# Kernel tuning notes

Measured on AMD Instinct MI355X. Metric: run time of the kernel, lower is better.

Reference implementation:

```python
import jax, jax.numpy as jnp
import numpy as np

B, L, E, V, H, M, O = 16, 64, 256, 16000, 8, 4, 2
DH = E // H
START = 0

def _pe():
    pos = np.arange(L, dtype=np.float32)[:, None]
    div = np.exp(np.arange(0, E, 2, dtype=np.float32) * (-np.log(10000.0) / E))
    pe = np.zeros((L, E), dtype=np.float32)
    pe[:, 0::2] = np.sin(pos * div)
    pe[:, 1::2] = np.cos(pos * div)
    return jnp.asarray(pe)

PE = _pe()  # [L, E] sinusoidal positional encoding (dropout p=0.0)


def setup_inputs() -> dict:
    key = jax.random.key(0)
    ks = jax.random.split(key, 16)
    g = lambda k, sh, sc: jax.random.normal(k, sh, jnp.float32) * sc
    return {
        'noise': jax.random.normal(ks[0], (B, L), jnp.float32),
        'inEmb_W': g(ks[1], (M, L, L), 1.0 / np.sqrt(L)),   # M stacked Linear(L, L), [in,out] layout
        'inEmb_b': jnp.zeros((M, L), jnp.float32),
        'Wq': g(ks[2], (O, E, E), 1.0 / np.sqrt(E)),
        'bq': jnp.zeros((O, E), jnp.float32),
        'Wk': g(ks[3], (O, E, E), 1.0 / np.sqrt(E)),
        'bk': jnp.zeros((O, E), jnp.float32),
        'Wv': g(ks[4], (O, E, E), 1.0 / np.sqrt(E)),
        'bv': jnp.zeros((O, E), jnp.float32),
        'Wo': g(ks[5], (O, E, E), 1.0 / np.sqrt(E)),
        'bo': jnp.zeros((O, E), jnp.float32),
        'ln_g': jnp.ones((O, E), jnp.float32),
        'ln_b': jnp.zeros((O, E), jnp.float32),
        'emb': g(ks[6], (V, E), 1.0),                       # Word2Vec embedding table
        'soft_W': g(ks[7], (E, V), 1.0 / np.sqrt(E)),       # soft head Linear(E, V)
        'soft_b': jnp.zeros((V,), jnp.float32),
    }


def _ln(x, g, b):
    mu = x.mean(-1, keepdims=True)
    var = ((x - mu) ** 2).mean(-1, keepdims=True)
    return (x - mu) / jnp.sqrt(var + 1e-5) * g + b


def _mha_norm(kv, q, Wq, bq, Wk, bk, Wv, bv, Wo, bo, g, b, kmask):
    # MHAwithNorm: attn(query=q, key=kv, value=kv) -> out proj -> residual -> LayerNorm
    Q = (q @ Wq + bq).reshape(B, L, H, DH)
    K = (kv @ Wk + bk).reshape(B, L, H, DH)
    Vh = (kv @ Wv + bv).reshape(B, L, H, DH)
    s = jnp.einsum('bqhd,bkhd->bhqk', Q, K) / np.sqrt(DH)
    s = jnp.where(kmask[None, None, None, :], s, -1e9)  # only the tok generated positions are valid keys
    a = jax.nn.softmax(s, axis=-1)
    o = jnp.einsum('bhqk,bkhd->bqhd', a, Vh).reshape(B, L, E)
    return _ln(o @ Wo + bo + q, g, b)


def _decode(noise, inEmb_W, inEmb_b, Wq, bq, Wk, bk, Wv, bv, Wo, bo, ln_g, ln_b, emb, soft_W, soft_b):
    w = noise
    for i in range(M):
        w = w @ inEmb_W[i] + inEmb_b[i]
    w = jnp.broadcast_to(w[:, :, None], (B, L, E))  # unsqueeze(-1).repeat(1,1,E)

    Y0 = jnp.zeros((B, L, E), jnp.float32).at[:, 0].set(emb[START] + PE[0])

    def step(Y, tok):
        kmask = jnp.arange(L) < tok  # current sequence length == tok
        out = Y
        for i in range(O):  # cross-attn blocks against w[:, :tok]
            out = _mha_norm(w, out, Wq[i], bq[i], Wk[i], bk[i], Wv[i], bv[i], Wo[i], bo[i], ln_g[i], ln_b[i], kmask)
        for i in range(O):  # same blocks reused as self-attn (faithful to source)
            out = _mha_norm(out, out, Wq[i], bq[i], Wk[i], bk[i], Wv[i], bv[i], Wo[i], bo[i], ln_g[i], ln_b[i], kmask)
        logits = out[:, tok - 1] @ soft_W + soft_b
        probs = jax.nn.softmax(logits, axis=-1)
        nxt = jnp.argmax(probs, axis=-1)  # [B]
        Y = Y.at[:, tok].set(emb[nxt] + PE[tok])
        return Y, (nxt, probs)

    _, (toks, probs) = jax.lax.scan(step, Y0, jnp.arange(1, L))
    return toks, probs  # toks [L-1, B] int, probs [L-1, B, V]


def reference(noise, inEmb_W, inEmb_b, Wq, bq, Wk, bk, Wv, bv, Wo, bo, ln_g, ln_b, emb, soft_W, soft_b):
    toks, _ = _decode(noise, inEmb_W, inEmb_b, Wq, bq, Wk, bk, Wv, bv, Wo, bo, ln_g, ln_b, emb, soft_W, soft_b)
    # torch.stack(out_sent[0]): generated token ids of batch element 0, incl. <START>
    return jnp.concatenate([jnp.array([START], dtype=toks.dtype), toks[:, 0]])
```

## Files before the change

### kernel.cpp

```cpp
#include <hip/hip_runtime.h>
#include <stdint.h>


#define NWG 128
#define NT 256

typedef unsigned long long ull;

__device__ __forceinline__ float ld_c(const float* p){
  return __hip_atomic_load(p, __ATOMIC_RELAXED, __HIP_MEMORY_SCOPE_AGENT);
}
__device__ __forceinline__ void st_c(float* p, float v){
  __hip_atomic_store(p, v, __ATOMIC_RELAXED, __HIP_MEMORY_SCOPE_AGENT);
}
__device__ __forceinline__ int ld_fi(const int* p){
  return __hip_atomic_load(p, __ATOMIC_RELAXED, __HIP_MEMORY_SCOPE_AGENT);
}
__device__ __forceinline__ void st_fi(int* p, int v){
  __hip_atomic_store(p, v, __ATOMIC_RELAXED, __HIP_MEMORY_SCOPE_AGENT);
}
__device__ __forceinline__ ull ld_u64(const ull* p){
  return __hip_atomic_load(p, __ATOMIC_RELAXED, __HIP_MEMORY_SCOPE_AGENT);
}
__device__ __forceinline__ void st_u64(ull* p, ull v){
  __hip_atomic_store(p, v, __ATOMIC_RELAXED, __HIP_MEMORY_SCOPE_AGENT);
}

__device__ __forceinline__ float wredsum(float v){
#pragma unroll
  for (int m=32;m;m>>=1) v += __shfl_xor(v,m,64);
  return v;
}
__device__ __forceinline__ float wredmax(float v){
#pragma unroll
  for (int m=32;m;m>>=1) v = fmaxf(v,__shfl_xor(v,m,64));
  return v;
}
__device__ __forceinline__ float g32sum(float v){
#pragma unroll
  for (int m=16;m;m>>=1) v += __shfl_xor(v,m,64);
  return v;
}
__device__ __forceinline__ float g32max(float v){
#pragma unroll
  for (int m=16;m;m>>=1) v = fmaxf(v,__shfl_xor(v,m,64));
  return v;
}
__device__ __forceinline__ ull shflx64(ull v,int m){
  unsigned int lo=(unsigned int)(v&0xffffffffull), hi=(unsigned int)(v>>32);
  lo=__shfl_xor(lo,m,64); hi=__shfl_xor(hi,m,64);
  return (((ull)hi)<<32)|(ull)lo;
}

__device__ __forceinline__ float pe_val(int l, int e){
  int j = e >> 1;
  float dv = expf((float)(2*j) * (-0.035977892078031970f));
  float arg = (float)l * dv;
  return (e & 1) ? cosf(arg) : sinf(arg);
}

__device__ __forceinline__ void a_chain(const float* xrow, float* rrow,
    float* m8, float* redv,
    const float* KAP, const float* BETA, const float* WVEC,
    const float* CC, const float* UT,
    const float* lng, const float* lnb, int tokm, int t){
  const float ISQ = 0.17677669529663687f;
  for (int blk=0; blk<2; blk++){
    const float* src = blk ? rrow : xrow;
    int hh=t>>5, j=t&31;
    float part=0.f;
    for (int jj=j; jj<256; jj+=32) part += src[jj]*KAP[(blk*8+hh)*256+jj];
    part = g32sum(part);
    float alpha = (part + BETA[blk*8+hh]) * ISQ;
    float s1 = (j<tokm)     ? alpha*WVEC[j]    : -3.4e38f;
    float s2 = (j+32<tokm)  ? alpha*WVEC[j+32] : -3.4e38f;
    float mx = g32max(fmaxf(s1,s2));
    float e1 = expf(s1-mx), e2 = expf(s2-mx);
    float sn = e1*((j<tokm)?WVEC[j]:0.f) + e2*((j+32<tokm)?WVEC[j+32]:0.f);
    float sd = e1+e2;
    sn=g32sum(sn); sd=g32sum(sd);
    if (j==0) m8[hh]=sn/sd;
    __syncthreads();
    float x_ = blk ? rrow[t] : xrow[t];
    float z = CC[blk*256+t] + x_;
#pragma unroll
    for (int h2=0;h2<8;h2++) z += m8[h2]*UT[(blk*8+h2)*256+t];
    float ssum=wredsum(z), ssq=wredsum(z*z);
    int lane=t&63, wid=t>>6;
    if (lane==0){ redv[wid]=ssum; redv[4+wid]=ssq; }
    __syncthreads();
    float ts=redv[0]+redv[1]+redv[2]+redv[3];
    float tq=redv[4]+redv[5]+redv[6]+redv[7];
    float mu=ts*(1.f/256.f);
    float var=tq*(1.f/256.f)-mu*mu;
    float rstd=1.f/sqrtf(var+1e-5f);
    float rv=(z-mu)*rstd*lng[blk*256+t]+lnb[blk*256+t];
    __syncthreads();
    rrow[t]=rv;
    __syncthreads();
  }
}

__device__ __forceinline__ void gbar_f(int* arr, int* rel, int ep){
  __syncthreads();
  if (threadIdx.x==0){
    __builtin_amdgcn_fence(__ATOMIC_RELEASE, "agent");
    __hip_atomic_store(arr + blockIdx.x*16, ep, __ATOMIC_RELAXED, __HIP_MEMORY_SCOPE_AGENT);
  }
  if (blockIdx.x==0){
    if (threadIdx.x < NWG){
      while (__hip_atomic_load(arr + threadIdx.x*16, __ATOMIC_RELAXED, __HIP_MEMORY_SCOPE_AGENT) != ep)
        __builtin_amdgcn_s_sleep(1);
    }
    __syncthreads();
    if (threadIdx.x==0)
      __hip_atomic_store(rel, ep, __ATOMIC_RELAXED, __HIP_MEMORY_SCOPE_AGENT);
  }
  if (threadIdx.x==0){
    while (__hip_atomic_load(rel, __ATOMIC_RELAXED, __HIP_MEMORY_SCOPE_AGENT) != ep)
      __builtin_amdgcn_s_sleep(1);
    __builtin_amdgcn_fence(__ATOMIC_ACQUIRE, "agent");
  }
  __syncthreads();
}

__device__ __forceinline__ void gbar_nf3(int* arr, int* relv, int ep){
  __syncthreads();
  if (threadIdx.x==0)
    st_fi(arr + blockIdx.x*16, ep);
  if (blockIdx.x==0){
    if (threadIdx.x < NWG){
      while (ld_fi(arr + threadIdx.x*16) != ep) __builtin_amdgcn_s_sleep(1);
    }
    __syncthreads();
    if (threadIdx.x < NWG) st_fi(relv + threadIdx.x*16, ep);
  }
  if (threadIdx.x==0){
    while (ld_fi(relv + blockIdx.x*16) != ep) __builtin_amdgcn_s_sleep(1);
  }
  __syncthreads();
}

extern "C" __global__ __launch_bounds__(256, 2)
void gen18124_kernel(const float* __restrict__ noise,
                     const float* __restrict__ iw, const float* __restrict__ ib,
                     const float* __restrict__ Wq, const float* __restrict__ bq,
                     const float* __restrict__ Wk, const float* __restrict__ bk,
                     const float* __restrict__ Wv, const float* __restrict__ bv,
                     const float* __restrict__ Wo, const float* __restrict__ bo,
                     const float* __restrict__ lng, const float* __restrict__ lnb,
                     const float* __restrict__ emb, const float* __restrict__ sw,
                     const float* __restrict__ sb,
                     int* __restrict__ out, float* __restrict__ ws)
{
  const float ISQ = 0.17677669529663687f;
  __shared__ float sm[5376];
  __shared__ ull redU[4];
  __shared__ int winS;
  __shared__ int wms;
  extern __shared__ float swl[];

  float* WVEC = ws;
  float* SKC  = ws+64;
  float* SVC  = ws+576;
  float* KAP  = ws+1088;
  float* UT   = ws+5184;
  float* CC   = ws+9280;
  float* BETA = ws+9792;
  int* ARR = (int*)(ws+10080);
  int* REL = (int*)(ws+12128);
  ull* KEY = (ull*)(ws+12160);
  float* Yg  = ws+14208;
  float* R1  = ws+30592;
  float* QB  = ws+46976;
  float* KB  = ws+63360;
  float* VB  = ws+79744;
  float* R2  = ws+96128;
  float* Z2P = ws+112512;
  float* Z3P = ws+243584;
  int* RELV  = (int*)(ws+245632);
  int* RELV2 = (int*)(ws+247680);
  int* Z3F2  = (int*)(ws+249728);

  const int g = blockIdx.x, t = threadIdx.x;
  int ep = 0;

  {
    const int base = g*125;
#pragma unroll 8
    for (int i=t; i<256*128; i+=NT){
      int e=i>>7, c=i&127;
      float val = 0.f;
      if (c<125) val = sw[e*16000 + base + c];
      swl[i]=val;
    }
  }

  {
    int c0 = 2*g;
    float a0=Wk[t*256+c0],       a1=Wk[t*256+c0+1];
    float a2=Wk[65536+t*256+c0], a3=Wk[65536+t*256+c0+1];
    float a4=Wv[t*256+c0],       a5=Wv[t*256+c0+1];
    float a6=Wv[65536+t*256+c0], a7=Wv[65536+t*256+c0+1];
    a0=wredsum(a0); a1=wredsum(a1); a2=wredsum(a2); a3=wredsum(a3);
    a4=wredsum(a4); a5=wredsum(a5); a6=wredsum(a6); a7=wredsum(a7);
    int lane=t&63, wid=t>>6;
    if (lane==0){
      sm[wid*8+0]=a0; sm[wid*8+1]=a1; sm[wid*8+2]=a2; sm[wid*8+3]=a3;
      sm[wid*8+4]=a4; sm[wid*8+5]=a5; sm[wid*8+6]=a6; sm[wid*8+7]=a7;
    }
    __syncthreads();
    if (t<8){
      float s=sm[t]+sm[8+t]+sm[16+t]+sm[24+t];
      if (t<4) SKC[(t>>1)*256 + c0 + (t&1)] = s;
      else     SVC[((t-4)>>1)*256 + c0 + ((t-4)&1)] = s;
    }
    __syncthreads();
    if (g==0){
      for (int i=t;i<16384;i+=NT) Z3F2[i]=0;
      float* wl = sm+64;
      if (t<64) wl[t] = noise[t];
      __syncthreads();
      for (int i=0;i<4;i++){
        float acc=0.f;
        if (t<64){
          for (int in_=0;in_<64;in_++) acc += wl[in_]*iw[(i*64+in_)*64+t];
          acc += ib[i*64+t];
        }
        __syncthreads();
        if (t<64) wl[t]=acc;
        __syncthreads();
      }
      if (t<64) WVEC[t]=wl[t];
    }
    if (g==1){
      Yg[t] = emb[t] + pe_val(0,t);
      if (t==0) out[0]=0;
    }
  }
  gbar_f(ARR,REL,++ep);

  {
    int c0 = 2*g;
    float p00 = bv[t]    *Wo[t*256+c0],        p01 = bv[t]    *Wo[t*256+c0+1];
    float p10 = bv[256+t]*Wo[65536+t*256+c0],  p11 = bv[256+t]*Wo[65536+t*256+c0+1];
    p00=wredsum(p00); p01=wredsum(p01); p10=wredsum(p10); p11=wredsum(p11);
    int lane=t&63, wid=t>>6;
    if (lane==0){ sm[wid*4+0]=p00; sm[wid*4+1]=p01; sm[wid*4+2]=p10; sm[wid*4+3]=p11; }
    __syncthreads();
    if (t<4){
      float s=sm[t]+sm[4+t]+sm[8+t]+sm[12+t];
      int i=t>>1, cl=t&1;
      CC[i*256+c0+cl] = s + bo[i*256+c0+cl];
    }
    if (t<32){
      int i=t>>4, h2=(t>>1)&7, c=c0+(t&1);
      float s=0.f;
      for (int e2=0;e2<32;e2++) s += SVC[i*256+h2*32+e2]*Wo[i*65536+(h2*32+e2)*256+c];
      UT[(i*8+h2)*256+c]=s;
    }
    if (t>=32 && t<64){
      int u=t-32, i=u>>4, h2=(u>>1)&7, e=c0+(u&1);
      float s=0.f;
      for (int c2=0;c2<32;c2++) s += Wq[i*65536+e*256+h2*32+c2]*SKC[i*256+h2*32+c2];
      KAP[(i*8+h2)*256+e]=s;
    }
    if (g==0 && t>=64 && t<80){
      int u=t-64, i=u>>3, h2=u&7;
      float s=0.f;
      for (int c2=0;c2<32;c2++) s += bq[i*256+h2*32+c2]*SKC[i*256+h2*32+c2];
      BETA[i*8+h2]=s;
    }
  }
  gbar_f(ARR,REL,++ep);

  if (g==0){
    float* axr=sm; float* arr=sm+256; float* am8=sm+512; float* ard=sm+528;
    axr[t]=ld_c(&Yg[t]);
    __syncthreads();
    a_chain(axr,arr,am8,ard, KAP,BETA,WVEC,CC,UT,lng,lnb, 1, t);
    st_c(&R1[t], arr[t]);
  }
  gbar_f(ARR,REL,++ep);

  const int h  = g&7;
  const int rg = g>>3;

  for (int tok=1; tok<64; tok++){
    const int n = tok-1;

    {
      float* rows4 = sm;
#pragma unroll
      for (int jj=0;jj<4;jj++) rows4[jj*256+t] = ld_c(&R1[(rg+16*jj)*256+t]);
      if (tok>1 && rg==(n&15)){
        float* axr=sm+2700; float* arr2=sm+2956; float* am8=sm+3212; float* ard=sm+3224;
        int v = winS;
        if (h==0 && t==0) out[n]=v;
        axr[t] = emb[v*256+t] + pe_val(n,t);
        if (h==0) st_c(&Yg[n*256+t], axr[t]);
        __syncthreads();
        a_chain(axr,arr2,am8,ard, KAP,BETA,WVEC,CC,UT,lng,lnb, tok, t);
        rows4[(n>>4)*256+t] = arr2[t];
        if (h==0) st_c(&R1[n*256+t], arr2[t]);
      }
      __syncthreads();
      int c=t&31, epp=t>>5;
      const int col=h*32+c;
      float aq[4]={0,0,0,0}, ak[4]={0,0,0,0}, av[4]={0,0,0,0};
#pragma unroll 8
      for (int e=epp*32; e<epp*32+32; e++){
        float wq_=Wq[e*256+col], wk_=Wk[e*256+col], wv_=Wv[e*256+col];
#pragma unroll
        for (int jj=0;jj<4;jj++){ float r=rows4[jj*256+e]; aq[jj]+=r*wq_; ak[jj]+=r*wk_; av[jj]+=r*wv_; }
      }
#pragma unroll
      for (int jj=0;jj<4;jj++){
        aq[jj]+=__shfl_xor(aq[jj],32,64);
        ak[jj]+=__shfl_xor(ak[jj],32,64);
        av[jj]+=__shfl_xor(av[jj],32,64);
      }
      float4* redq=(float4*)(sm+1056); float4* redk=(float4*)(sm+1568); float4* redv4=(float4*)(sm+2080);
      int lane=t&63, wid=t>>6;
      if (lane<32){
        redq[wid*32+lane]=make_float4(aq[0],aq[1],aq[2],aq[3]);
        redk[wid*32+lane]=make_float4(ak[0],ak[1],ak[2],ak[3]);
        redv4[wid*32+lane]=make_float4(av[0],av[1],av[2],av[3]);
      }
      __syncthreads();
      if (t<32){
        float4 A=redq[t],B4=redq[32+t],C4=redq[64+t],D4=redq[96+t];
        float sq[4]={A.x+B4.x+C4.x+D4.x, A.y+B4.y+C4.y+D4.y, A.z+B4.z+C4.z+D4.z, A.w+B4.w+C4.w+D4.w};
        A=redk[t];B4=redk[32+t];C4=redk[64+t];D4=redk[96+t];
        float sk[4]={A.x+B4.x+C4.x+D4.x, A.y+B4.y+C4.y+D4.y, A.z+B4.z+C4.z+D4.z, A.w+B4.w+C4.w+D4.w};
        A=redv4[t];B4=redv4[32+t];C4=redv4[64+t];D4=redv4[96+t];
        float sv[4]={A.x+B4.x+C4.x+D4.x, A.y+B4.y+C4.y+D4.y, A.z+B4.z+C4.z+D4.z, A.w+B4.w+C4.w+D4.w};
        int cc=h*32+t;
        float bq_=bq[cc], bk_=bk[cc], bv_=bv[cc];
#pragma unroll
        for (int jj=0;jj<4;jj++){
          int q_=rg+16*jj;
          if (q_<tok){
            st_c(&QB[q_*256+cc], sq[jj]+bq_);
            st_c(&KB[q_*256+cc], sk[jj]+bk_);
            st_c(&VB[q_*256+cc], sv[jj]+bv_);
          }
        }
      }
    }
    gbar_nf3(ARR,RELV,++ep);

    {
      float* Ks=sm; float* Vs=sm+2112; float* qrow=sm+4224; float* arow=sm+4352; float* o2s=sm+4608;
      int k=t>>2, f0=(t&3)*8;
      if (k<tok){
#pragma unroll
        for (int i2=0;i2<8;i2++){
          Ks[k*33+f0+i2]=ld_c(&KB[k*256+h*32+f0+i2]);
          Vs[k*33+f0+i2]=ld_c(&VB[k*256+h*32+f0+i2]);
        }
      }
      if (t<128){ int jj=t>>5, c=t&31; int q_=rg+16*jj; if (q_<tok) qrow[jj*32+c]=ld_c(&QB[q_*256+h*32+c]); }
      __syncthreads();
      int w=t>>6, lane=t&63; int q_=rg+16*w; bool ok=q_<tok;
      float sc=-3.4e38f;
      if (ok && lane<tok){
        sc=0.f;
#pragma unroll
        for (int c2=0;c2<32;c2++) sc+=qrow[w*32+c2]*Ks[lane*33+c2];
        sc*=ISQ;
      }
      float mx=wredmax(sc);
      float ex=(ok&&lane<tok)? expf(sc-mx):0.f;
      float sd=wredsum(ex);
      arow[w*64+lane]= ok ? ex/sd : 0.f;
      __syncthreads();
      int j=lane&31, half=lane>>5;
      float oa=0.f;
      if (ok){ for (int k2=half;k2<tok;k2+=2) oa+=arow[w*64+k2]*Vs[k2*33+j]; }
      oa += __shfl_xor(oa,32,64);
      if (lane<32) o2s[w*32+j]=oa;
      __syncthreads();
      float acc[4]={0,0,0,0};
#pragma unroll 8
      for (int j2=0;j2<32;j2++){
        float wv_=Wo[(h*32+j2)*256+t];
#pragma unroll
        for (int jj=0;jj<4;jj++) acc[jj]+=o2s[jj*32+j2]*wv_;
      }
#pragma unroll
      for (int jj=0;jj<4;jj++){ int q2=rg+16*jj; if (q2<tok) st_c(&Z2P[(h*64+q2)*256+t], acc[jj]); }
    }
    gbar_nf3(ARR,RELV,++ep);

    {
      float* rows4=sm; float* mus=sm+1024;
#pragma unroll
      for (int jj=0;jj<4;jj++){
        int q_=rg+16*jj;
        float z = bo[t] + ld_c(&R1[q_*256+t]);
#pragma unroll
        for (int h2=0;h2<8;h2++) z += ld_c(&Z2P[(h2*64+q_)*256+t]);
        rows4[jj*256+t]=z;
      }
      __syncthreads();
      {
        int w=t>>6, lane=t&63;
        float v0=rows4[w*256+lane], v1=rows4[w*256+64+lane], v2=rows4[w*256+128+lane], v3=rows4[w*256+192+lane];
        float s=v0+v1+v2+v3, sq2=v0*v0+v1*v1+v2*v2+v3*v3;
        s=wredsum(s); sq2=wredsum(sq2);
        if (lane==0){
          float mu=s*(1.f/256.f);
          float var=sq2*(1.f/256.f)-mu*mu;
          mus[w*2]=mu; mus[w*2+1]=1.f/sqrtf(var+1e-5f);
        }
      }
      __syncthreads();
#pragma unroll
      for (int jj=0;jj<4;jj++){
        float mu=mus[jj*2], rstd=mus[jj*2+1];
        float val=(rows4[jj*256+t]-mu)*rstd*lng[t]+lnb[t];
        rows4[jj*256+t]=val;
        int q_=rg+16*jj;
        if (h==0 && q_==n) st_c(&R2[q_*256+t], val);
      }
      __syncthreads();
      int c=t&31, epp=t>>5;
      const int col=h*32+c;
      float aq[4]={0,0,0,0}, ak[4]={0,0,0,0}, av[4]={0,0,0,0};
#pragma unroll 8
      for (int e=epp*32; e<epp*32+32; e++){
        float wq_=Wq[65536+e*256+col], wk_=Wk[65536+e*256+col], wv_=Wv[65536+e*256+col];
#pragma unroll
        for (int jj=0;jj<4;jj++){ float r=rows4[jj*256+e]; aq[jj]+=r*wq_; ak[jj]+=r*wk_; av[jj]+=r*wv_; }
      }
#pragma unroll
      for (int jj=0;jj<4;jj++){
        aq[jj]+=__shfl_xor(aq[jj],32,64);
        ak[jj]+=__shfl_xor(ak[jj],32,64);
        av[jj]+=__shfl_xor(av[jj],32,64);
      }
      float4* redq=(float4*)(sm+1056); float4* redk=(float4*)(sm+1568); float4* redv4=(float4*)(sm+2080);
      int lane=t&63, wid=t>>6;
      if (lane<32){
        redq[wid*32+lane]=make_float4(aq[0],aq[1],aq[2],aq[3]);
        redk[wid*32+lane]=make_float4(ak[0],ak[1],ak[2],ak[3]);
        redv4[wid*32+lane]=make_float4(av[0],av[1],av[2],av[3]);
      }
      __syncthreads();
      if (t<32){
        float4 A=redq[t],B4=redq[32+t],C4=redq[64+t],D4=redq[96+t];
        float sq[4]={A.x+B4.x+C4.x+D4.x, A.y+B4.y+C4.y+D4.y, A.z+B4.z+C4.z+D4.z, A.w+B4.w+C4.w+D4.w};
        A=redk[t];B4=redk[32+t];C4=redk[64+t];D4=redk[96+t];
        float sk[4]={A.x+B4.x+C4.x+D4.x, A.y+B4.y+C4.y+D4.y, A.z+B4.z+C4.z+D4.z, A.w+B4.w+C4.w+D4.w};
        A=redv4[t];B4=redv4[32+t];C4=redv4[64+t];D4=redv4[96+t];
        float sv[4]={A.x+B4.x+C4.x+D4.x, A.y+B4.y+C4.y+D4.y, A.z+B4.z+C4.z+D4.z, A.w+B4.w+C4.w+D4.w};
        int cc=h*32+t;
#pragma unroll
        for (int jj=0;jj<4;jj++){
          int q_=rg+16*jj;
          if (q_<tok){
            st_c(&KB[q_*256+cc], sk[jj]+bk[256+cc]);
            st_c(&VB[q_*256+cc], sv[jj]+bv[256+cc]);
            if (q_==n) st_c(&QB[q_*256+cc], sq[jj]+bq[256+cc]);
          }
        }
      }
    }
    gbar_nf3(ARR,RELV,++ep);

    {
      float resid = ld_c(&R2[n*256+t]);
      if (g < 8){
        const int hh = g;
        float* Ks=sm; float* Vs=sm+2112; float* qn=sm+4224; float* arow=sm+4352; float* o3s=sm+4608;
        int k=t>>2, f0=(t&3)*8;
        if (k<tok){
#pragma unroll
          for (int i2=0;i2<8;i2++){
            Ks[k*33+f0+i2]=ld_c(&KB[k*256+hh*32+f0+i2]);
            Vs[k*33+f0+i2]=ld_c(&VB[k*256+hh*32+f0+i2]);
          }
        }
        if (t<32) qn[t]=ld_c(&QB[n*256+hh*32+t]);
        __syncthreads();
        int lane=t&63, w=t>>6;
        if (w==0){
          float sc=-3.4e38f;
          if (lane<tok){
            sc=0.f;
#pragma unroll
            for (int c2=0;c2<32;c2++) sc+=qn[c2]*Ks[lane*33+c2];
            sc*=ISQ;
          }
          float mx=wredmax(sc);
          float ex=(lane<tok)? expf(sc-mx):0.f;
          float sd=wredsum(ex);
          arow[lane]=ex/sd;
        }
        __syncthreads();
        if (w==0){
          int j=lane&31, half=lane>>5;
          float oa=0.f;
          for (int k2=half;k2<tok;k2+=2) oa+=arow[k2]*Vs[k2*33+j];
          oa+=__shfl_xor(oa,32,64);
          if (lane<32) o3s[j]=oa;
        }
        __syncthreads();
        float acc=0.f;
#pragma unroll 8
        for (int j2=0;j2<32;j2++) acc+=o3s[j2]*Wo[65536+(hh*32+j2)*256+t];
        st_c(&Z3P[hh*256+t], acc);
        __syncthreads();
        if (t < NWG) st_fi(Z3F2 + (hh*NWG + t)*16, tok);
      } else if (g>=64 && g<127){
        const int q = g-64;
        if (q < tok && tok < 63){
          float* axr=sm; float* arr2=sm+256; float* am8=sm+512; float* ard=sm+528;
          axr[t]=ld_c(&Yg[q*256+t]);
          __syncthreads();
          a_chain(axr,arr2,am8,ard, KAP,BETA,WVEC,CC,UT,lng,lnb, tok+1, t);
          st_c(&R1[q*256+t], arr2[t]);
        }
      }
      if (t<8){ while (ld_fi(Z3F2 + (t*NWG + g)*16) < tok) __builtin_amdgcn_s_sleep(1); }
      __syncthreads();
      float* outn=sm; float* redv=sm+256; float* pp=sm+512;
      float z = bo[256+t] + resid;
#pragma unroll
      for (int h2=0;h2<8;h2++) z += ld_c(&Z3P[h2*256+t]);
      float s=wredsum(z), sq2=wredsum(z*z);
      int lane=t&63, wid=t>>6;
      if (lane==0){ redv[wid]=s; redv[4+wid]=sq2; }
      __syncthreads();
      float ts=redv[0]+redv[1]+redv[2]+redv[3];
      float tq=redv[4]+redv[5]+redv[6]+redv[7];
      float mu=ts*(1.f/256.f);
      float var=tq*(1.f/256.f)-mu*mu;
      float rstd=1.f/sqrtf(var+1e-5f);
      outn[t]=(z-mu)*rstd*lng[256+t]+lnb[256+t];
      __syncthreads();
      const int c = t & 127, half = t >> 7;
      float acc = 0.f;
      if (c < 125){
        const int e0 = half*128;
#pragma unroll 8
        for (int e=e0; e<e0+128; e++) acc += outn[e]*swl[e*128+c];
      }
      if (half==1 && c<125) pp[c]=acc;
      __syncthreads();
      ull key=0ull;
      if (half==0 && c<125){
        int v=g*125+c;
        float a2 = acc + pp[c] + sb[v];
        unsigned int fb=__float_as_uint(a2);
        fb = (fb&0x80000000u)? ~fb : (fb|0x80000000u);
        key=(((ull)fb)<<32) | (ull)(~(unsigned int)v);
      }
#pragma unroll
      for (int m=32;m;m>>=1){
        ull o=shflx64(key,m);
        key = (o>key)? o : key;
      }
      if (lane==0) redU[wid]=key;
      __syncthreads();
      if (t==0){
        ull kk=redU[0];
        if (redU[1]>kk) kk=redU[1];
        if (redU[2]>kk) kk=redU[2];
        if (redU[3]>kk) kk=redU[3];
        st_u64(KEY + g*8, kk);
      }
    }
    {
      ++ep;
      __syncthreads();
      if (t==0)
        st_fi(ARR + g*16, ep);
      if (g==0){
        if (t < NWG){
          while (ld_fi(ARR + t*16) != ep) __builtin_amdgcn_s_sleep(1);
        }
        __syncthreads();
        ull k = 0ull;
        if (t < NWG) k = ld_u64(KEY + t*8);
#pragma unroll
        for (int m=32;m;m>>=1){
          ull o=shflx64(k,m);
          k = (o>k)? o : k;
        }
        if ((t&63)==0) redU[t>>6]=k;
        __syncthreads();
        if (t==0){
          ull kk=redU[0];
          if (redU[1]>kk) kk=redU[1];
          wms = (int)(~(unsigned int)(kk & 0xffffffffull));
        }
        __syncthreads();
        if (t < NWG) st_fi(RELV2 + t*16, (ep<<14) | wms);
      }
      if (t==0){
        int r;
        while (((r = ld_fi(RELV2 + g*16)) >> 14) != ep) __builtin_amdgcn_s_sleep(1);
        winS = r & 0x3fff;
      }
      __syncthreads();
    }
  }

  if (g==0 && t==0) out[63] = winS;
}

extern "C" void kernel_launch(void* const* d_in, const int* in_sizes, int n_in,
                              void* d_out, int out_size, void* d_ws, size_t ws_size,
                              hipStream_t stream)
{
  (void)in_sizes; (void)n_in; (void)out_size; (void)ws_size;
  hipLaunchKernelGGL(gen18124_kernel, dim3(NWG), dim3(NT), 131072, stream,
    (const float*)d_in[0],  (const float*)d_in[1],  (const float*)d_in[2],
    (const float*)d_in[3],  (const float*)d_in[4],  (const float*)d_in[5],
    (const float*)d_in[6],  (const float*)d_in[7],  (const float*)d_in[8],
    (const float*)d_in[9],  (const float*)d_in[10], (const float*)d_in[11],
    (const float*)d_in[12], (const float*)d_in[13], (const float*)d_in[14],
    (const float*)d_in[15], (int*)d_out, (float*)d_ws);
}
```

Baseline: 4.032 ms.

## Add dedicated coordinator workgroup for grid barriers and argmax reduction

Launches one extra workgroup that acts as the barrier master for the four grid barriers per decode token. It busy-spins without sleeping and also does the global argmax key reduction and broadcast. Worker block 0 no longer does this master work, so it drops off the critical path, and workers now just signal arrival and wait for their release flag. The cost is a permanently spinning extra workgroup. The barrier arrays are also shifted so the larger arrival array does not overlap the release slot.

```diff
diff --git a/kernel.cpp b/kernel.cpp
--- a/kernel.cpp
+++ b/kernel.cpp
@@ -2,7 +2,8 @@
 #include <stdint.h>
 
 
-#define NWG 128
+#define NWG 129
+#define NWRK 128
 #define NT 256
 
 typedef unsigned long long ull;
@@ -124,18 +125,10 @@
   __syncthreads();
 }
 
-__device__ __forceinline__ void gbar_nf3(int* arr, int* relv, int ep){
+__device__ __forceinline__ void gbar_w(int* arr, int* relv, int ep){
   __syncthreads();
-  if (threadIdx.x==0)
+  if (threadIdx.x==0){
     st_fi(arr + blockIdx.x*16, ep);
-  if (blockIdx.x==0){
-    if (threadIdx.x < NWG){
-      while (ld_fi(arr + threadIdx.x*16) != ep) __builtin_amdgcn_s_sleep(1);
-    }
-    __syncthreads();
-    if (threadIdx.x < NWG) st_fi(relv + threadIdx.x*16, ep);
-  }
-  if (threadIdx.x==0){
     while (ld_fi(relv + blockIdx.x*16) != ep) __builtin_amdgcn_s_sleep(1);
   }
   __syncthreads();
@@ -168,7 +161,7 @@
   float* CC   = ws+9280;
   float* BETA = ws+9792;
   int* ARR = (int*)(ws+10080);
-  int* REL = (int*)(ws+12128);
+  int* REL = (int*)(ws+12144);
   ull* KEY = (ull*)(ws+12160);
   float* Yg  = ws+14208;
   float* R1  = ws+30592;
@@ -185,7 +178,7 @@
   const int g = blockIdx.x, t = threadIdx.x;
   int ep = 0;
 
-  {
+  if (g < NWRK){
     const int base = g*125;
 #pragma unroll 8
     for (int i=t; i<256*128; i+=NT){
@@ -196,7 +189,7 @@
     }
   }
 
-  {
+  if (g < NWRK){
     int c0 = 2*g;
     float a0=Wk[t*256+c0],       a1=Wk[t*256+c0+1];
     float a2=Wk[65536+t*256+c0], a3=Wk[65536+t*256+c0+1];
@@ -240,7 +233,7 @@
   }
   gbar_f(ARR,REL,++ep);
 
-  {
+  if (g < NWRK){
     int c0 = 2*g;
     float p00 = bv[t]    *Wo[t*256+c0],        p01 = bv[t]    *Wo[t*256+c0+1];
     float p10 = bv[256+t]*Wo[65536+t*256+c0],  p11 = bv[256+t]*Wo[65536+t*256+c0+1];
@@ -282,6 +275,39 @@
     st_c(&R1[t], arr[t]);
   }
   gbar_f(ARR,REL,++ep);
+
+  if (g == NWRK){
+    for (int tok=1; tok<64; tok++){
+      for (int b=0;b<3;b++){
+        ++ep;
+        if (t < NWRK){ while (ld_fi(ARR + t*16) != ep) {} }
+        __syncthreads();
+        if (t < NWRK) st_fi(RELV + t*16, ep);
+        __syncthreads();
+      }
+      ++ep;
+      if (t < NWRK){ while (ld_fi(ARR + t*16) != ep) {} }
+      __syncthreads();
+      ull k = 0ull;
+      if (t < NWRK) k = ld_u64(KEY + t*8);
+#pragma unroll
+      for (int m=32;m;m>>=1){
+        ull o=shflx64(k,m);
+        k = (o>k)? o : k;
+      }
+      if ((t&63)==0 && t<NWRK) redU[t>>6]=k;
+      __syncthreads();
+      if (t==0){
+        ull kk=redU[0];
+        if (redU[1]>kk) kk=redU[1];
+        wms = (int)(~(unsigned int)(kk & 0xffffffffull));
+      }
+      __syncthreads();
+      if (t < NWRK) st_fi(RELV2 + t*16, (ep<<14) | wms);
+      __syncthreads();
+    }
+    return;
+  }
 
   const int h  = g&7;
   const int rg = g>>3;
@@ -348,7 +374,7 @@
         }
       }
     }
-    gbar_nf3(ARR,RELV,++ep);
+    gbar_w(ARR,RELV,++ep);
 
     {
       float* Ks=sm; float* Vs=sm+2112; float* qrow=sm+4224; float* arow=sm+4352; float* o2s=sm+4608;
@@ -391,7 +417,7 @@
 #pragma unroll
       for (int jj=0;jj<4;jj++){ int q2=rg+16*jj; if (q2<tok) st_c(&Z2P[(h*64+q2)*256+t], acc[jj]); }
     }
-    gbar_nf3(ARR,RELV,++ep);
+    gbar_w(ARR,RELV,++ep);
 
     {
       float* rows4=sm; float* mus=sm+1024;
@@ -467,7 +493,7 @@
         }
       }
     }
-    gbar_nf3(ARR,RELV,++ep);
+    gbar_w(ARR,RELV,++ep);
 
     {
       float resid = ld_c(&R2[n*256+t]);
@@ -512,7 +538,7 @@
         for (int j2=0;j2<32;j2++) acc+=o3s[j2]*Wo[65536+(hh*32+j2)*256+t];
         st_c(&Z3P[hh*256+t], acc);
         __syncthreads();
-        if (t < NWG) st_fi(Z3F2 + (hh*NWG + t)*16, tok);
+        if (t < NWRK) st_fi(Z3F2 + (hh*NWRK + t)*16, tok);
       } else if (g>=64 && g<127){
         const int q = g-64;
         if (q < tok && tok < 63){
@@ -523,7 +549,7 @@
           st_c(&R1[q*256+t], arr2[t]);
         }
       }
-      if (t<8){ while (ld_fi(Z3F2 + (t*NWG + g)*16) < tok) __builtin_amdgcn_s_sleep(1); }
+      if (t<8){ while (ld_fi(Z3F2 + (t*NWRK + g)*16) < tok) __builtin_amdgcn_s_sleep(1); }
       __syncthreads();
       float* outn=sm; float* redv=sm+256; float* pp=sm+512;
       float z = bo[256+t] + resid;
@@ -575,31 +601,8 @@
     {
       ++ep;
       __syncthreads();
-      if (t==0)
+      if (t==0){
         st_fi(ARR + g*16, ep);
-      if (g==0){
-        if (t < NWG){
-          while (ld_fi(ARR + t*16) != ep) __builtin_amdgcn_s_sleep(1);
-        }
-        __syncthreads();
-        ull k = 0ull;
-        if (t < NWG) k = ld_u64(KEY + t*8);
-#pragma unroll
-        for (int m=32;m;m>>=1){
-          ull o=shflx64(k,m);
-          k = (o>k)? o : k;
-        }
-        if ((t&63)==0) redU[t>>6]=k;
-        __syncthreads();
-        if (t==0){
-          ull kk=redU[0];
-          if (redU[1]>kk) kk=redU[1];
-          wms = (int)(~(unsigned int)(kk & 0xffffffffull));
-        }
-        __syncthreads();
-        if (t < NWG) st_fi(RELV2 + t*16, (ep<<14) | wms);
-      }
-      if (t==0){
         int r;
         while (((r = ld_fi(RELV2 + g*16)) >> 14) != ep) __builtin_amdgcn_s_sleep(1);
         winS = r & 0x3fff;
```

Measured after the change: 4.050 ms. About the same (+0.4%).
